# Performance work log

Hardware: AMD Instinct MI355X
Metric: run time of the kernel (lower is better)

The kernel has to match this reference:

```python
import jax, jax.numpy as jnp
from jax import lax
import numpy as np

ALPHA = 0.1  # topological regularization weight
INF = jnp.float32(1e30)


def _delay_embed(x):
    # Takens time-delay embedding, dimension 3, delay 1: [L] -> [L-2, 3]
    return jnp.stack([x[:-2], x[1:-1], x[2:]], axis=-1)


def _pdist(p):
    # Euclidean pairwise distances: [n,3] -> [n,n]
    sq = jnp.sum(p * p, axis=-1)
    d2 = sq[:, None] + sq[None, :] - 2.0 * (p @ p.T)
    return jnp.sqrt(jnp.maximum(d2, 0.0))


def _mst_deaths(D):
    # 0-dimensional Vietoris-Rips persistence death times = single-linkage
    # merge heights = MST edge weights. Dense Prim, O(n^2), sequential pairing
    # phase mirrors the per-sample CPU persistent-homology loop of the original.
    n = D.shape[0]
    visited = jnp.zeros((n,), dtype=bool).at[0].set(True)
    mind = D[0].at[0].set(INF)  # min distance from tree to each vertex
    deaths = jnp.zeros((n - 1,), dtype=D.dtype)

    def body(i, carry):
        mind, visited, deaths = carry
        cand = jnp.where(visited, INF, mind)
        j = jnp.argmin(cand)
        deaths = deaths.at[i].set(cand[j])
        visited = visited.at[j].set(True)
        mind = jnp.minimum(mind, D[j])
        return (mind, visited, deaths)

    _, _, deaths = lax.fori_loop(0, n - 1, body, (mind, visited, deaths))
    return deaths


def _topo_features(x):
    # x: [B, L] -> sorted (descending) persistence values per sample: [B, L-3]
    def one(series):
        D = _pdist(_delay_embed(series))
        return jnp.sort(_mst_deaths(D))[::-1]
    return jax.vmap(one)(x)


def setup_inputs() -> dict:
    key = jax.random.key(0)
    k1, k2 = jax.random.split(key)
    B, L = 32, 2048
    pred = jax.random.normal(k1, (B, L), dtype=jnp.float32)
    target = jax.random.normal(k2, (B, L), dtype=jnp.float32)
    return {"pred": pred, "target": target}


def reference(pred, target):
    mse_loss = jnp.mean((pred - target) ** 2)
    # topological features are computed on detached data in the original
    pred_topo = lax.stop_gradient(_topo_features(pred))
    target_topo = lax.stop_gradient(_topo_features(target))
    topo_loss = jnp.mean((pred_topo - target_topo) ** 2)
    return mse_loss + ALPHA * topo_loss
```

## Files before the change

### kernel.cpp

```cpp
#include <hip/hip_runtime.h>
#include <math.h>

#define LLEN 2048
#define BATCH 32
#define N_PTS (LLEN - 2)
#define N_DEATH (LLEN - 3)
#define SORT_N 2048
#define TPB 256
#define PT 8
#define NW 4
#define BIG 1e30f
#define TOPO_BYTES ((size_t)64 * N_DEATH * 4)

typedef float v2f __attribute__((ext_vector_type(2)));

__device__ __forceinline__ unsigned dpp_umin6(unsigned v) {
    unsigned t;
    t = (unsigned)__builtin_amdgcn_update_dpp(-1, (int)v, 0x111, 0xF, 0xF, false);
    v = t < v ? t : v;
    t = (unsigned)__builtin_amdgcn_update_dpp(-1, (int)v, 0x112, 0xF, 0xF, false);
    v = t < v ? t : v;
    t = (unsigned)__builtin_amdgcn_update_dpp(-1, (int)v, 0x114, 0xF, 0xF, false);
    v = t < v ? t : v;
    t = (unsigned)__builtin_amdgcn_update_dpp(-1, (int)v, 0x118, 0xF, 0xF, false);
    v = t < v ? t : v;
    t = (unsigned)__builtin_amdgcn_update_dpp(-1, (int)v, 0x142, 0xF, 0xF, false);
    v = t < v ? t : v;
    t = (unsigned)__builtin_amdgcn_update_dpp(-1, (int)v, 0x143, 0xF, 0xF, false);
    v = t < v ? t : v;
    return v;
}

__global__ __launch_bounds__(TPB)
void topo_kernel(const float* __restrict__ pred,
                 const float* __restrict__ tgt,
                 float* __restrict__ topo ,
                 unsigned* __restrict__ ctr,
                 int fuse,
                 float* __restrict__ out) {
    __shared__ float4 pp[SORT_N];
    __shared__ float deaths[SORT_N];
    __shared__ __align__(16) unsigned xslot[2 * NW];
    __shared__ unsigned lastflag;

    const int b = blockIdx.x;
    const float* x = (b < BATCH) ? (pred + b * LLEN) : (tgt + (b - BATCH) * LLEN);
    const int t = threadIdx.x;
    const int lane = t & 63;
    const int wid = t >> 6;

    v2f px2[PT / 2], py2[PT / 2], pz2[PT / 2];
    unsigned m[PT];
    unsigned idxs[PT];
    unsigned vis = 0;
#pragma unroll
    for (int s = 0; s < PT; ++s) {
        int idx = t * PT + s;
        idxs[s] = (unsigned)idx;
        bool valid = idx < N_PTS;
        float vx = valid ? x[idx]     : 0.f;
        float vy = valid ? x[idx + 1] : 0.f;
        float vz = valid ? x[idx + 2] : 0.f;
        if (s & 1) { px2[s >> 1].y = vx; py2[s >> 1].y = vy; pz2[s >> 1].y = vz; }
        else       { px2[s >> 1].x = vx; py2[s >> 1].x = vy; pz2[s >> 1].x = vz; }
        pp[idx] = make_float4(vx, vy, vz, 0.f);
        m[s] = 0x7F800000u | idxs[s];
        if (!valid || idx == 0) vis |= 1u << s;
    }
    __syncthreads();

    float pjx = x[0], pjy = x[1], pjz = x[2];

    for (int i = 0; i < N_DEATH; ++i) {
        v2f jx = {pjx, pjx}, jy = {pjy, pjy}, jz = {pjz, pjz};
        unsigned lv0 = 0xFFFFFFFFu, lv1 = 0xFFFFFFFFu;
#pragma unroll
        for (int k = 0; k < PT / 2; ++k) {
            v2f dx = px2[k] - jx, dy = py2[k] - jy, dz = pz2[k] - jz;
            v2f d2 = dx * dx + dy * dy + dz * dz;
            unsigned pk0 = (__float_as_uint(d2.x) & 0xFFFFF000u) | idxs[2 * k];
            unsigned pk1 = (__float_as_uint(d2.y) & 0xFFFFF000u) | idxs[2 * k + 1];
            unsigned nm0 = m[2 * k] < pk0 ? m[2 * k] : pk0;
            unsigned nm1 = m[2 * k + 1] < pk1 ? m[2 * k + 1] : pk1;
            m[2 * k] = nm0;
            m[2 * k + 1] = nm1;
            unsigned e0 = (unsigned)__builtin_amdgcn_sbfe((int)vis, 2 * k, 1);
            unsigned e1 = (unsigned)__builtin_amdgcn_sbfe((int)vis, 2 * k + 1, 1);
            unsigned c0 = nm0 | e0, c1 = nm1 | e1;
            lv0 = lv0 < c0 ? lv0 : c0;
            lv1 = lv1 < c1 ? lv1 : c1;
        }
        unsigned lv = lv0 < lv1 ? lv0 : lv1;
        unsigned wmin = dpp_umin6(lv);
        const int base = (i & 1) * NW;
        if (lane == 63) xslot[base + wid] = wmin;
        asm volatile("s_barrier" ::: "memory");
        const uint4 q = *(const uint4*)&xslot[base];
        unsigned w01 = q.x < q.y ? q.x : q.y;
        unsigned w23 = q.z < q.w ? q.z : q.w;
        unsigned win = w01 < w23 ? w01 : w23;
        int j = (int)(win & 0x7FFu);
        vis |= (t == (j >> 3)) ? (1u << (j & 7)) : 0u;
        float4 pj = pp[j];
        pjx = pj.x; pjy = pj.y; pjz = pj.z;
        if (t == 0) deaths[i] = __uint_as_float(win & 0xFFFFF000u);
    }

    if (t < SORT_N - N_DEATH) deaths[N_DEATH + t] = -BIG;
    __syncthreads();

    for (int k = 2; k <= SORT_N; k <<= 1) {
        for (int jj = k >> 1; jj > 0; jj >>= 1) {
#pragma unroll
            for (int s = 0; s < SORT_N / TPB; ++s) {
                int ii = t + s * TPB;
                int ixj = ii ^ jj;
                if (ixj > ii) {
                    float a = deaths[ii], c = deaths[ixj];
                    bool descBlock = ((ii & k) == 0);
                    bool doSwap = descBlock ? (a < c) : (a > c);
                    if (doSwap) { deaths[ii] = c; deaths[ixj] = a; }
                }
            }
            __syncthreads();
        }
    }

    for (int e = t; e < N_DEATH; e += TPB)
        topo[b * N_DEATH + e] = sqrtf(deaths[e]);

    if (!fuse) return;

    __syncthreads();
    if (t == 0) {
        __threadfence();
        unsigned prev = __hip_atomic_fetch_add(ctr, 1u, __ATOMIC_ACQ_REL,
                                               __HIP_MEMORY_SCOPE_AGENT);
        lastflag = (prev == 63u) ? 1u : 0u;
        __threadfence();
    }
    __syncthreads();
    if (lastflag == 0u) return;

    float msum = 0.f;
    const float4* p4 = (const float4*)pred;
    const float4* t4 = (const float4*)tgt;
    for (int e = t; e < (BATCH * LLEN) / 4; e += TPB) {
        float4 a = p4[e], c = t4[e];
        float dx = a.x - c.x, dy = a.y - c.y, dz = a.z - c.z, dw = a.w - c.w;
        msum += dx * dx + dy * dy + dz * dz + dw * dw;
    }
    float tsum = 0.f;
    const float4* q4 = (const float4*)topo;
    const int nt4 = (BATCH * N_DEATH) / 4;
    for (int e = t; e < nt4; e += TPB) {
        float4 a = q4[e], c = q4[e + nt4];
        float dx = a.x - c.x, dy = a.y - c.y, dz = a.z - c.z, dw = a.w - c.w;
        tsum += dx * dx + dy * dy + dz * dz + dw * dw;
    }
    __shared__ float sm[2][NW];
#pragma unroll
    for (int off = 32; off >= 1; off >>= 1) {
        msum += __shfl_xor(msum, off);
        tsum += __shfl_xor(tsum, off);
    }
    if (lane == 0) { sm[0][wid] = msum; sm[1][wid] = tsum; }
    __syncthreads();
    if (t == 0) {
        float M = 0.f, T = 0.f;
#pragma unroll
        for (int w = 0; w < NW; ++w) { M += sm[0][w]; T += sm[1][w]; }
        out[0] = M / (float)(BATCH * LLEN) + 0.1f * (T / (float)(BATCH * N_DEATH));
    }
}

#define RTPB 1024
__global__ __launch_bounds__(RTPB)
void loss_kernel(const float* __restrict__ pred,
                 const float* __restrict__ tgt,
                 const float* __restrict__ topo,
                 float* __restrict__ out) {
    const int t = threadIdx.x;
    float msum = 0.f;
    const float4* p4 = (const float4*)pred;
    const float4* t4 = (const float4*)tgt;
    const int n4 = (BATCH * LLEN) / 4;
    for (int e = t; e < n4; e += RTPB) {
        float4 a = p4[e], c = t4[e];
        float dx = a.x - c.x, dy = a.y - c.y, dz = a.z - c.z, dw = a.w - c.w;
        msum += dx * dx + dy * dy + dz * dz + dw * dw;
    }
    float tsum = 0.f;
    const int nt = BATCH * N_DEATH;
    for (int e = t; e < nt; e += RTPB) {
        float d = topo[e] - topo[e + nt];
        tsum += d * d;
    }
    __shared__ float sm[2][RTPB / 64];
#pragma unroll
    for (int off = 32; off >= 1; off >>= 1) {
        msum += __shfl_xor(msum, off);
        tsum += __shfl_xor(tsum, off);
    }
    int lane = t & 63, wid = t >> 6;
    if (lane == 0) { sm[0][wid] = msum; sm[1][wid] = tsum; }
    __syncthreads();
    if (t == 0) {
        float M = 0.f, T = 0.f;
#pragma unroll
        for (int w = 0; w < RTPB / 64; ++w) { M += sm[0][w]; T += sm[1][w]; }
        out[0] = M / (float)(BATCH * LLEN) + 0.1f * (T / (float)nt);
    }
}

extern "C" void kernel_launch(void* const* d_in, const int* in_sizes, int n_in,
                              void* d_out, int out_size, void* d_ws, size_t ws_size,
                              hipStream_t stream) {
    const float* pred = (const float*)d_in[0];
    const float* tgt  = (const float*)d_in[1];
    float* topo = (float*)d_ws;
    unsigned* ctr = (unsigned*)((char*)d_ws + TOPO_BYTES);
    const int fuse = (ws_size >= TOPO_BYTES + sizeof(unsigned)) ? 1 : 0;

    if (fuse) hipMemsetAsync(ctr, 0, sizeof(unsigned), stream);

    topo_kernel<<<2 * BATCH, TPB, 0, stream>>>(pred, tgt, topo,
                                               fuse ? ctr : nullptr, fuse,
                                               (float*)d_out);
    if (!fuse)
        loss_kernel<<<1, RTPB, 0, stream>>>(pred, tgt, topo, (float*)d_out);
}
```

Measured before the change: 708.9 us.

## Run Prim loop in a single wave with staged active-set compaction

Moves the sequential Prim MST loop from four waves with a per-step block barrier to a single wave that broadcasts the argmin via readlane. The work is split into phases that compact unvisited points (carrying their current min distances) into LDS, so later phases scan fewer points per lane. This removes barrier and cross-wave LDS traffic per step, but serializes the early phases' ALU work onto one SIMD with many points per lane, raising register pressure.

```diff
diff --git a/kernel.cpp b/kernel.cpp
--- a/kernel.cpp
+++ b/kernel.cpp
@@ -7,7 +7,6 @@
 #define N_DEATH (LLEN - 3)
 #define SORT_N 2048
 #define TPB 256
-#define PT 8
 #define NW 4
 #define BIG 1e30f
 #define TOPO_BYTES ((size_t)64 * N_DEATH * 4)
@@ -29,6 +28,86 @@
     t = (unsigned)__builtin_amdgcn_update_dpp(-1, (int)v, 0x143, 0xF, 0xF, false);
     v = t < v ? t : v;
     return v;
+}
+
+template<int K, bool FIRST, bool COMPACT>
+__device__ __forceinline__ void solo_phase(const int lane, const int i0, const int i1,
+                                           float4* pp, float* deaths,
+                                           float& pjx, float& pjy, float& pjz) {
+    v2f px2[K / 2], py2[K / 2], pz2[K / 2];
+    unsigned m[K], idxs[K];
+    unsigned vis = 0u;
+#pragma unroll
+    for (int r = 0; r < K; ++r) {
+        const int slot = r * 64 + lane;
+        idxs[r] = (unsigned)slot;
+        float4 p = pp[slot];
+        if (r & 1) { px2[r >> 1].y = p.x; py2[r >> 1].y = p.y; pz2[r >> 1].y = p.z; }
+        else       { px2[r >> 1].x = p.x; py2[r >> 1].x = p.y; pz2[r >> 1].x = p.z; }
+        if (FIRST) m[r] = 0x7F800000u | (unsigned)slot;
+        else       m[r] = __float_as_uint(p.w);
+    }
+    if (FIRST) {
+        if (lane == 0) vis |= 1u;
+#pragma unroll
+        for (int r = 0; r < K; ++r)
+            if (r * 64 + lane >= N_PTS) vis |= 1u << r;
+    }
+
+#pragma unroll 1
+    for (int i = i0; i < i1; ++i) {
+        v2f jx = {pjx, pjx}, jy = {pjy, pjy}, jz = {pjz, pjz};
+        unsigned lv0 = 0xFFFFFFFFu, lv1 = 0xFFFFFFFFu;
+        unsigned lv2 = 0xFFFFFFFFu, lv3 = 0xFFFFFFFFu;
+#pragma unroll
+        for (int k2 = 0; k2 < K / 2; ++k2) {
+            v2f dx = px2[k2] - jx, dy = py2[k2] - jy, dz = pz2[k2] - jz;
+            v2f d2 = dx * dx + dy * dy + dz * dz;
+            unsigned pk0 = (__float_as_uint(d2.x) & 0xFFFFF000u) | idxs[2 * k2];
+            unsigned pk1 = (__float_as_uint(d2.y) & 0xFFFFF000u) | idxs[2 * k2 + 1];
+            unsigned nm0 = m[2 * k2] < pk0 ? m[2 * k2] : pk0;
+            unsigned nm1 = m[2 * k2 + 1] < pk1 ? m[2 * k2 + 1] : pk1;
+            m[2 * k2] = nm0;
+            m[2 * k2 + 1] = nm1;
+            unsigned e0 = (unsigned)__builtin_amdgcn_sbfe((int)vis, 2 * k2, 1);
+            unsigned e1 = (unsigned)__builtin_amdgcn_sbfe((int)vis, 2 * k2 + 1, 1);
+            unsigned c0 = nm0 | e0, c1 = nm1 | e1;
+            if ((k2 & 1) == 0) { lv0 = lv0 < c0 ? lv0 : c0; lv1 = lv1 < c1 ? lv1 : c1; }
+            else               { lv2 = lv2 < c0 ? lv2 : c0; lv3 = lv3 < c1 ? lv3 : c1; }
+        }
+        unsigned lva = lv0 < lv1 ? lv0 : lv1;
+        unsigned lvb = lv2 < lv3 ? lv2 : lv3;
+        unsigned lv = lva < lvb ? lva : lvb;
+        unsigned wmin = dpp_umin6(lv);
+        unsigned w = (unsigned)__builtin_amdgcn_readlane((int)wmin, 63);
+        int j = (int)(w & 0x7FFu);
+        if (lane == (j & 63)) vis |= 1u << (j >> 6);
+        float4 pj = pp[j];
+        pjx = pj.x; pjy = pj.y; pjz = pj.z;
+        if (lane == 0) deaths[i] = __uint_as_float(w & 0xFFFFF000u);
+    }
+
+    if (COMPACT) {
+        unsigned ucnt = (unsigned)K - (unsigned)__popc(vis);
+        unsigned inc = ucnt;
+#pragma unroll
+        for (int d = 1; d < 64; d <<= 1) {
+            unsigned tt = (unsigned)__shfl_up((int)inc, d, 64);
+            if (lane >= d) inc += tt;
+        }
+        unsigned base = inc - ucnt;
+#pragma unroll
+        for (int r = 0; r < K; ++r) {
+            if (!((vis >> r) & 1u)) {
+                float xx = (r & 1) ? px2[r >> 1].y : px2[r >> 1].x;
+                float yy = (r & 1) ? py2[r >> 1].y : py2[r >> 1].x;
+                float zz = (r & 1) ? pz2[r >> 1].y : pz2[r >> 1].x;
+                pp[base] = make_float4(xx, yy, zz,
+                                       __uint_as_float((m[r] & 0xFFFFF000u) | base));
+                ++base;
+            }
+        }
+    }
 }
 
 __global__ __launch_bounds__(TPB)
@@ -40,7 +119,6 @@
                  float* __restrict__ out) {
     __shared__ float4 pp[SORT_N];
     __shared__ float deaths[SORT_N];
-    __shared__ __align__(16) unsigned xslot[2 * NW];
     __shared__ unsigned lastflag;
 
     const int b = blockIdx.x;
@@ -49,63 +127,29 @@
     const int lane = t & 63;
     const int wid = t >> 6;
 
-    v2f px2[PT / 2], py2[PT / 2], pz2[PT / 2];
-    unsigned m[PT];
-    unsigned idxs[PT];
-    unsigned vis = 0;
-#pragma unroll
-    for (int s = 0; s < PT; ++s) {
-        int idx = t * PT + s;
-        idxs[s] = (unsigned)idx;
+#pragma unroll
+    for (int s = 0; s < 8; ++s) {
+        int idx = t * 8 + s;
         bool valid = idx < N_PTS;
         float vx = valid ? x[idx]     : 0.f;
         float vy = valid ? x[idx + 1] : 0.f;
         float vz = valid ? x[idx + 2] : 0.f;
-        if (s & 1) { px2[s >> 1].y = vx; py2[s >> 1].y = vy; pz2[s >> 1].y = vz; }
-        else       { px2[s >> 1].x = vx; py2[s >> 1].x = vy; pz2[s >> 1].x = vz; }
         pp[idx] = make_float4(vx, vy, vz, 0.f);
-        m[s] = 0x7F800000u | idxs[s];
-        if (!valid || idx == 0) vis |= 1u << s;
-    }
-    __syncthreads();
-
-    float pjx = x[0], pjy = x[1], pjz = x[2];
-
-    for (int i = 0; i < N_DEATH; ++i) {
-        v2f jx = {pjx, pjx}, jy = {pjy, pjy}, jz = {pjz, pjz};
-        unsigned lv0 = 0xFFFFFFFFu, lv1 = 0xFFFFFFFFu;
-#pragma unroll
-        for (int k = 0; k < PT / 2; ++k) {
-            v2f dx = px2[k] - jx, dy = py2[k] - jy, dz = pz2[k] - jz;
-            v2f d2 = dx * dx + dy * dy + dz * dz;
-            unsigned pk0 = (__float_as_uint(d2.x) & 0xFFFFF000u) | idxs[2 * k];
-            unsigned pk1 = (__float_as_uint(d2.y) & 0xFFFFF000u) | idxs[2 * k + 1];
-            unsigned nm0 = m[2 * k] < pk0 ? m[2 * k] : pk0;
-            unsigned nm1 = m[2 * k + 1] < pk1 ? m[2 * k + 1] : pk1;
-            m[2 * k] = nm0;
-            m[2 * k + 1] = nm1;
-            unsigned e0 = (unsigned)__builtin_amdgcn_sbfe((int)vis, 2 * k, 1);
-            unsigned e1 = (unsigned)__builtin_amdgcn_sbfe((int)vis, 2 * k + 1, 1);
-            unsigned c0 = nm0 | e0, c1 = nm1 | e1;
-            lv0 = lv0 < c0 ? lv0 : c0;
-            lv1 = lv1 < c1 ? lv1 : c1;
-        }
-        unsigned lv = lv0 < lv1 ? lv0 : lv1;
-        unsigned wmin = dpp_umin6(lv);
-        const int base = (i & 1) * NW;
-        if (lane == 63) xslot[base + wid] = wmin;
-        asm volatile("s_barrier" ::: "memory");
-        const uint4 q = *(const uint4*)&xslot[base];
-        unsigned w01 = q.x < q.y ? q.x : q.y;
-        unsigned w23 = q.z < q.w ? q.z : q.w;
-        unsigned win = w01 < w23 ? w01 : w23;
-        int j = (int)(win & 0x7FFu);
-        vis |= (t == (j >> 3)) ? (1u << (j & 7)) : 0u;
-        float4 pj = pp[j];
-        pjx = pj.x; pjy = pj.y; pjz = pj.z;
-        if (t == 0) deaths[i] = __uint_as_float(win & 0xFFFFF000u);
-    }
-
+    }
+    __syncthreads();
+
+    if (wid == 0) {
+        float4 p0 = pp[0];
+        float pjx = p0.x, pjy = p0.y, pjz = p0.z;
+        solo_phase<32, true,  true >(lane, 0,    509,  pp, deaths, pjx, pjy, pjz);
+        solo_phase<24, false, true >(lane, 509,  1021, pp, deaths, pjx, pjy, pjz);
+        solo_phase<16, false, true >(lane, 1021, 1277, pp, deaths, pjx, pjy, pjz);
+        solo_phase<12, false, true >(lane, 1277, 1533, pp, deaths, pjx, pjy, pjz);
+        solo_phase<8,  false, true >(lane, 1533, 1661, pp, deaths, pjx, pjy, pjz);
+        solo_phase<6,  false, true >(lane, 1661, 1789, pp, deaths, pjx, pjy, pjz);
+        solo_phase<4,  false, true >(lane, 1789, 1917, pp, deaths, pjx, pjy, pjz);
+        solo_phase<2,  false, false>(lane, 1917, 2045, pp, deaths, pjx, pjy, pjz);
+    }
     if (t < SORT_N - N_DEATH) deaths[N_DEATH + t] = -BIG;
     __syncthreads();
 
```

After: 903.5 us. 1.27x slower.

## Split Prim loop into phases that compact unvisited vertices to shrink per-thread work

Applied to the files above, without the earlier changes.

The sequential Prim loop now runs in four phases. At each phase boundary the still-unvisited vertices and their current min-distances are compacted into shared memory with a wave prefix scan. Each thread then handles 8, 6, 4 and finally 2 points per iteration instead of always 8, which cuts the distance/min arithmetic in later iterations. Points are laid out strided (s*256+t), and the packed index now refers to the compacted position. The compaction adds a few barriers and may change tie-breaking among equal keys.

```diff
diff --git a/kernel.cpp b/kernel.cpp
--- a/kernel.cpp
+++ b/kernel.cpp
@@ -7,7 +7,6 @@
 #define N_DEATH (LLEN - 3)
 #define SORT_N 2048
 #define TPB 256
-#define PT 8
 #define NW 4
 #define BIG 1e30f
 #define TOPO_BYTES ((size_t)64 * N_DEATH * 4)
@@ -29,6 +28,98 @@
     t = (unsigned)__builtin_amdgcn_update_dpp(-1, (int)v, 0x143, 0xF, 0xF, false);
     v = t < v ? t : v;
     return v;
+}
+
+template<int PT, bool FIRST, bool COMPACT>
+__device__ __forceinline__ void prim_phase(
+    const int t, const int lane, const int wid,
+    const int i0, const int i1, const unsigned rem_in,
+    float4* __restrict__ pp, float* __restrict__ deaths,
+    unsigned* __restrict__ xslot, unsigned* __restrict__ wtot,
+    float& pjx, float& pjy, float& pjz)
+{
+    v2f px2[PT / 2], py2[PT / 2], pz2[PT / 2];
+    unsigned m[PT];
+    unsigned vis = 0u;
+#pragma unroll
+    for (int s = 0; s < PT; ++s) {
+        const int idx = s * 256 + t;
+        float4 p = pp[idx];
+        if (s & 1) { px2[s >> 1].y = p.x; py2[s >> 1].y = p.y; pz2[s >> 1].y = p.z; }
+        else       { px2[s >> 1].x = p.x; py2[s >> 1].x = p.y; pz2[s >> 1].x = p.z; }
+        if (FIRST) {
+            m[s] = 0x7F800000u | (unsigned)idx;
+            if (idx >= (int)rem_in || idx == 0) vis |= 1u << s;
+        } else {
+            m[s] = __float_as_uint(p.w);
+            if (idx >= (int)rem_in) vis |= 1u << s;
+        }
+    }
+
+#pragma unroll 1
+    for (int i = i0; i < i1; ++i) {
+        v2f jx = {pjx, pjx}, jy = {pjy, pjy}, jz = {pjz, pjz};
+        unsigned lv0 = 0xFFFFFFFFu, lv1 = 0xFFFFFFFFu;
+#pragma unroll
+        for (int k = 0; k < PT / 2; ++k) {
+            v2f dx = px2[k] - jx, dy = py2[k] - jy, dz = pz2[k] - jz;
+            v2f d2 = dx * dx + dy * dy + dz * dz;
+            unsigned pk0 = (__float_as_uint(d2.x) & 0xFFFFF000u) | (unsigned)((2 * k) * 256 + t);
+            unsigned pk1 = (__float_as_uint(d2.y) & 0xFFFFF000u) | (unsigned)((2 * k + 1) * 256 + t);
+            unsigned nm0 = m[2 * k] < pk0 ? m[2 * k] : pk0;
+            unsigned nm1 = m[2 * k + 1] < pk1 ? m[2 * k + 1] : pk1;
+            m[2 * k] = nm0;
+            m[2 * k + 1] = nm1;
+            unsigned e0 = (unsigned)__builtin_amdgcn_sbfe((int)vis, 2 * k, 1);
+            unsigned e1 = (unsigned)__builtin_amdgcn_sbfe((int)vis, 2 * k + 1, 1);
+            unsigned c0 = nm0 | e0, c1 = nm1 | e1;
+            lv0 = lv0 < c0 ? lv0 : c0;
+            lv1 = lv1 < c1 ? lv1 : c1;
+        }
+        unsigned lv = lv0 < lv1 ? lv0 : lv1;
+        unsigned wmin = dpp_umin6(lv);
+        const int base = (i & 1) * NW;
+        if (lane == 63) xslot[base + wid] = wmin;
+        asm volatile("s_barrier" ::: "memory");
+        const uint4 q = *(const uint4*)&xslot[base];
+        unsigned w01 = q.x < q.y ? q.x : q.y;
+        unsigned w23 = q.z < q.w ? q.z : q.w;
+        unsigned win = w01 < w23 ? w01 : w23;
+        int j = (int)(win & 0x7FFu);
+        vis |= (t == (j & 255)) ? (1u << (j >> 8)) : 0u;
+        float4 pj = pp[j];
+        pjx = pj.x; pjy = pj.y; pjz = pj.z;
+        if (t == 0) deaths[i] = __uint_as_float(win & 0xFFFFF000u);
+    }
+
+    if (COMPACT) {
+        const unsigned livemask = ~vis & ((1u << PT) - 1u);
+        const unsigned cnt = (unsigned)__popc(livemask);
+        unsigned inc = cnt;
+#pragma unroll
+        for (int d = 1; d < 64; d <<= 1) {
+            unsigned tt = (unsigned)__shfl_up((int)inc, d, 64);
+            if (lane >= d) inc += tt;
+        }
+        if (lane == 63) wtot[wid] = inc;
+        asm volatile("s_barrier" ::: "memory");
+        unsigned wbase = 0;
+#pragma unroll
+        for (int w = 0; w < NW; ++w) wbase += (w < wid) ? wtot[w] : 0u;
+        unsigned dst = wbase + inc - cnt;
+#pragma unroll
+        for (int s = 0; s < PT; ++s) {
+            if ((livemask >> s) & 1u) {
+                float xx = (s & 1) ? px2[s >> 1].y : px2[s >> 1].x;
+                float yy = (s & 1) ? py2[s >> 1].y : py2[s >> 1].x;
+                float zz = (s & 1) ? pz2[s >> 1].y : pz2[s >> 1].x;
+                pp[dst] = make_float4(xx, yy, zz,
+                                      __uint_as_float((m[s] & 0xFFFFF000u) | dst));
+                ++dst;
+            }
+        }
+        asm volatile("s_barrier" ::: "memory");
+    }
 }
 
 __global__ __launch_bounds__(TPB)
@@ -41,6 +132,7 @@
     __shared__ float4 pp[SORT_N];
     __shared__ float deaths[SORT_N];
     __shared__ __align__(16) unsigned xslot[2 * NW];
+    __shared__ unsigned wtot[NW];
     __shared__ unsigned lastflag;
 
     const int b = blockIdx.x;
@@ -49,62 +141,23 @@
     const int lane = t & 63;
     const int wid = t >> 6;
 
-    v2f px2[PT / 2], py2[PT / 2], pz2[PT / 2];
-    unsigned m[PT];
-    unsigned idxs[PT];
-    unsigned vis = 0;
-#pragma unroll
-    for (int s = 0; s < PT; ++s) {
-        int idx = t * PT + s;
-        idxs[s] = (unsigned)idx;
+#pragma unroll
+    for (int s = 0; s < 8; ++s) {
+        int idx = s * 256 + t;
         bool valid = idx < N_PTS;
         float vx = valid ? x[idx]     : 0.f;
         float vy = valid ? x[idx + 1] : 0.f;
         float vz = valid ? x[idx + 2] : 0.f;
-        if (s & 1) { px2[s >> 1].y = vx; py2[s >> 1].y = vy; pz2[s >> 1].y = vz; }
-        else       { px2[s >> 1].x = vx; py2[s >> 1].x = vy; pz2[s >> 1].x = vz; }
         pp[idx] = make_float4(vx, vy, vz, 0.f);
-        m[s] = 0x7F800000u | idxs[s];
-        if (!valid || idx == 0) vis |= 1u << s;
     }
     __syncthreads();
 
     float pjx = x[0], pjy = x[1], pjz = x[2];
 
-    for (int i = 0; i < N_DEATH; ++i) {
-        v2f jx = {pjx, pjx}, jy = {pjy, pjy}, jz = {pjz, pjz};
-        unsigned lv0 = 0xFFFFFFFFu, lv1 = 0xFFFFFFFFu;
-#pragma unroll
-        for (int k = 0; k < PT / 2; ++k) {
-            v2f dx = px2[k] - jx, dy = py2[k] - jy, dz = pz2[k] - jz;
-            v2f d2 = dx * dx + dy * dy + dz * dz;
-            unsigned pk0 = (__float_as_uint(d2.x) & 0xFFFFF000u) | idxs[2 * k];
-            unsigned pk1 = (__float_as_uint(d2.y) & 0xFFFFF000u) | idxs[2 * k + 1];
-            unsigned nm0 = m[2 * k] < pk0 ? m[2 * k] : pk0;
-            unsigned nm1 = m[2 * k + 1] < pk1 ? m[2 * k + 1] : pk1;
-            m[2 * k] = nm0;
-            m[2 * k + 1] = nm1;
-            unsigned e0 = (unsigned)__builtin_amdgcn_sbfe((int)vis, 2 * k, 1);
-            unsigned e1 = (unsigned)__builtin_amdgcn_sbfe((int)vis, 2 * k + 1, 1);
-            unsigned c0 = nm0 | e0, c1 = nm1 | e1;
-            lv0 = lv0 < c0 ? lv0 : c0;
-            lv1 = lv1 < c1 ? lv1 : c1;
-        }
-        unsigned lv = lv0 < lv1 ? lv0 : lv1;
-        unsigned wmin = dpp_umin6(lv);
-        const int base = (i & 1) * NW;
-        if (lane == 63) xslot[base + wid] = wmin;
-        asm volatile("s_barrier" ::: "memory");
-        const uint4 q = *(const uint4*)&xslot[base];
-        unsigned w01 = q.x < q.y ? q.x : q.y;
-        unsigned w23 = q.z < q.w ? q.z : q.w;
-        unsigned win = w01 < w23 ? w01 : w23;
-        int j = (int)(win & 0x7FFu);
-        vis |= (t == (j >> 3)) ? (1u << (j & 7)) : 0u;
-        float4 pj = pp[j];
-        pjx = pj.x; pjy = pj.y; pjz = pj.z;
-        if (t == 0) deaths[i] = __uint_as_float(win & 0xFFFFF000u);
-    }
+    prim_phase<8, true,  true >(t, lane, wid, 0,    509,  N_PTS, pp, deaths, xslot, wtot, pjx, pjy, pjz);
+    prim_phase<6, false, true >(t, lane, wid, 509,  1021, 1536,  pp, deaths, xslot, wtot, pjx, pjy, pjz);
+    prim_phase<4, false, true >(t, lane, wid, 1021, 1533, 1024,  pp, deaths, xslot, wtot, pjx, pjy, pjz);
+    prim_phase<2, false, false>(t, lane, wid, 1533, 2045, 512,   pp, deaths, xslot, wtot, pjx, pjy, pjz);
 
     if (t < SORT_N - N_DEATH) deaths[N_DEATH + t] = -BIG;
     __syncthreads();
```

New measurement: 631.3 us, median of 2. -10.9%, faster.
